# Kernel tuning notes

Measured on AMD Instinct MI355X. Metric: run time of the kernel, lower is better.

## Reference

```python
import jax, jax.numpy as jnp
import numpy as np

DIM = 768
HEADS = 12
HEAD_DIM = DIM // HEADS


def setup_inputs() -> dict:
    key = jax.random.key(0)
    ks = jax.random.split(key, 5)
    s = 0.02
    return {
        "x": jax.random.normal(ks[0], (2, 4096, DIM), dtype=jnp.float32),
        "w_qkv": jax.random.normal(ks[1], (DIM, 3 * DIM), dtype=jnp.float32) * s,
        "b_qkv": jax.random.normal(ks[2], (3 * DIM,), dtype=jnp.float32) * s,
        "w_proj": jax.random.normal(ks[3], (DIM, DIM), dtype=jnp.float32) * s,
        "b_proj": jax.random.normal(ks[4], (DIM,), dtype=jnp.float32) * s,
    }


def reference(x, w_qkv, b_qkv, w_proj, b_proj):
    B, N, _ = x.shape
    scale = HEAD_DIM ** (-0.5)
    qkv = x @ w_qkv + b_qkv                              # [B, N, 3*DIM]
    q, k, v = jnp.split(qkv, 3, axis=-1)
    # 'b n (h d) -> b h n d'
    def to_heads(t):
        return t.reshape(B, N, HEADS, HEAD_DIM).transpose(0, 2, 1, 3)
    q, k, v = to_heads(q), to_heads(k), to_heads(v)
    attn = jnp.einsum('bhnd,bhmd->bhnm', q, k) * scale   # [B, H, N, N]
    attn = jax.nn.softmax(attn, axis=-1)
    out = jnp.einsum('bhnm,bhmd->bhnd', attn, v)         # [B, H, N, D]
    out = out.transpose(0, 2, 1, 3).reshape(B, N, DIM)   # 'b h n d -> b n (h d)'
    return out @ w_proj + b_proj
```

## Files before the change

kernel.cpp:

```cpp
#include <hip/hip_runtime.h>
#include <hip/hip_bf16.h>
#include <stdint.h>

typedef _Float16 f16x8 __attribute__((ext_vector_type(8)));
typedef _Float16 f16x4 __attribute__((ext_vector_type(4)));
typedef uint32_t u32x2 __attribute__((ext_vector_type(2)));
typedef float floatx4 __attribute__((ext_vector_type(4)));

#define NSEQ 4096
#define DIMM 768
#define NHEADS 12
#define HD 64

__device__ __forceinline__ void gload_lds16(const void* g, void* l) {
  typedef __attribute__((address_space(1))) const uint32_t GQ;
  typedef __attribute__((address_space(3))) uint32_t LQ;
  __builtin_amdgcn_global_load_lds((GQ*)g, (LQ*)l, 16, 0, 0);
}

__device__ __forceinline__ uint16_t f16_bits(float v) {
  _Float16 h = (_Float16)v;
  return __builtin_bit_cast(uint16_t, h);
}

__device__ __forceinline__ uint32_t pkrtz(float a, float b) {
  return __builtin_bit_cast(uint32_t, __builtin_amdgcn_cvt_pkrtz(a, b));
}

__device__ __forceinline__ int swz(int row, int e) {
  return row * 64 + ((((e >> 3) ^ (row & 7)) << 3) | (e & 7));
}

__global__ __launch_bounds__(256) void convert_f32_f16(
    const float4* __restrict__ src, f16x8* __restrict__ dst, int n8) {
  const int i = blockIdx.x * 256 + threadIdx.x;
  if (i >= n8) return;
  const float4 a = src[2 * i], b = src[2 * i + 1];
  f16x8 o;
  o[0] = (_Float16)a.x; o[1] = (_Float16)a.y; o[2] = (_Float16)a.z; o[3] = (_Float16)a.w;
  o[4] = (_Float16)b.x; o[5] = (_Float16)b.y; o[6] = (_Float16)b.z; o[7] = (_Float16)b.w;
  dst[i] = o;
}

__global__ __launch_bounds__(256) void transpose_f32_f16(
    const float* __restrict__ src, uint16_t* __restrict__ dst, int R, int C) {
  __shared__ uint16_t tile[32][33];
  const int c0 = blockIdx.x * 32, r0 = blockIdx.y * 32;
  const int tx = threadIdx.x, ty = threadIdx.y;
#pragma unroll
  for (int i = 0; i < 32; i += 8)
    tile[ty + i][tx] = f16_bits(src[(size_t)(r0 + ty + i) * C + (c0 + tx)]);
  __syncthreads();
#pragma unroll
  for (int i = 0; i < 32; i += 8)
    dst[(size_t)(c0 + ty + i) * R + (r0 + tx)] = tile[tx][ty + i];
}

__global__ __launch_bounds__(256) void transpose_b16(
    const uint16_t* __restrict__ src, uint16_t* __restrict__ dst, int R, int C) {
  __shared__ uint16_t tile[32][33];
  const size_t plane = (size_t)blockIdx.z * (size_t)R * (size_t)C;
  const int c0 = blockIdx.x * 32, r0 = blockIdx.y * 32;
  const int tx = threadIdx.x, ty = threadIdx.y;
#pragma unroll
  for (int i = 0; i < 32; i += 8)
    tile[ty + i][tx] = src[plane + (size_t)(r0 + ty + i) * C + (c0 + tx)];
  __syncthreads();
#pragma unroll
  for (int i = 0; i < 32; i += 8)
    dst[plane + (size_t)(c0 + ty + i) * R + (r0 + tx)] = tile[tx][ty + i];
}

__global__ __launch_bounds__(256) void gemm_bt(
    const _Float16* __restrict__ A, const _Float16* __restrict__ Bt,
    const float* __restrict__ bias, int K, int mode,
    void* __restrict__ o0, _Float16* __restrict__ o1, _Float16* __restrict__ o2) {
  __shared__ __attribute__((aligned(16))) _Float16 As[128 * 32];
  __shared__ __attribute__((aligned(16))) _Float16 Bs[128 * 32];
  __shared__ float bias_s[128];
  const int tid = threadIdx.x;
  const int wv = tid >> 6;
  const int lane = tid & 63;
  const int quad = lane >> 4, l16 = lane & 15;
  const int wm = (wv >> 1) * 64, wn = (wv & 1) * 64;
  const int m0 = blockIdx.y * 128, n0 = blockIdx.x * 128;

  if (tid < 128) bias_s[tid] = bias[n0 + tid];

  floatx4 acc[4][4];
#pragma unroll
  for (int i = 0; i < 4; ++i)
#pragma unroll
    for (int j = 0; j < 4; ++j) acc[i][j] = (floatx4){0.f, 0.f, 0.f, 0.f};

  const int gr = lane >> 2, gc = (lane & 3) * 8;
  const _Float16* Ag = A + (size_t)(m0 + wv * 32 + gr) * K + gc;
  const _Float16* Bg = Bt + (size_t)(n0 + wv * 32 + gr) * K + gc;
  const size_t K16 = (size_t)16 * K;
  _Float16* As0 = &As[wv * 1024];
  _Float16* Bs0 = &Bs[wv * 1024];

  for (int kt = 0; kt < K; kt += 32) {
    __syncthreads();
    gload_lds16(Ag + kt, As0);
    gload_lds16(Ag + kt + K16, As0 + 512);
    gload_lds16(Bg + kt, Bs0);
    gload_lds16(Bg + kt + K16, Bs0 + 512);
    __syncthreads();
    f16x8 af[4], bfr[4];
#pragma unroll
    for (int i = 0; i < 4; ++i)
      af[i] = *(const f16x8*)&As[(wm + i * 16 + l16) * 32 + quad * 8];
#pragma unroll
    for (int j = 0; j < 4; ++j)
      bfr[j] = *(const f16x8*)&Bs[(wn + j * 16 + l16) * 32 + quad * 8];
#pragma unroll
    for (int i = 0; i < 4; ++i)
#pragma unroll
      for (int j = 0; j < 4; ++j)
        acc[i][j] = __builtin_amdgcn_mfma_f32_16x16x32_f16(af[i], bfr[j], acc[i][j], 0, 0, 0);
  }

  if (mode == 0) {
    float* of = (float*)o0;
#pragma unroll
    for (int i = 0; i < 4; ++i)
#pragma unroll
      for (int j = 0; j < 4; ++j) {
        const int col = n0 + wn + j * 16 + l16;
        const float b = bias_s[wn + j * 16 + l16];
        const int mrow = m0 + wm + i * 16 + quad * 4;
#pragma unroll
        for (int r = 0; r < 4; ++r)
          of[(size_t)(mrow + r) * DIMM + col] = acc[i][j][r] + b;
      }
  } else {
    const int sec = n0 / DIMM;
    _Float16* dst = (sec == 0) ? (_Float16*)o0 : (sec == 1) ? o1 : o2;
    const float sc = (sec == 0) ? 0.18033688011112042f : 1.0f;
#pragma unroll
    for (int i = 0; i < 4; ++i)
#pragma unroll
      for (int j = 0; j < 4; ++j) {
        const int n = n0 + wn + j * 16 + l16;
        const int c = n - sec * DIMM;
        const int h = c >> 6, d = c & 63;
        const float b = bias_s[wn + j * 16 + l16];
        const int mrow = m0 + wm + i * 16 + quad * 4;
#pragma unroll
        for (int r = 0; r < 4; ++r) {
          const int m = mrow + r;
          const int bb = m >> 12, nr = m & 4095;
          dst[(((size_t)(bb * NHEADS + h)) * NSEQ + nr) * HD + d] =
              (_Float16)((acc[i][j][r] + b) * sc);
        }
      }
  }
}

__global__ __launch_bounds__(256, 3) void attn(
    const _Float16* __restrict__ Qg, const _Float16* __restrict__ Kg,
    const _Float16* __restrict__ VTg, _Float16* __restrict__ ctx) {
  __shared__ __attribute__((aligned(16))) _Float16 Pt[128 * 64];
  __shared__ __attribute__((aligned(16))) _Float16 Ks[2][64 * 64];
  __shared__ __attribute__((aligned(16))) _Float16 VTs[2][64 * 64];
  const int tid = threadIdx.x;
  const int wv = tid >> 6, lane = tid & 63;
  const int quad = lane >> 4, l16 = lane & 15;
  const int bi = blockIdx.x;
  const int xcd = bi & 7, j = bi >> 3;
  const int bh = xcd * 3 + (j >> 5);
  const int q0 = (j & 31) * 128;
  const int bb = bh / NHEADS, h = bh - bb * NHEADS;
  const _Float16* Qp = Qg + (size_t)bh * NSEQ * HD;
  const _Float16* Kp = Kg + (size_t)bh * NSEQ * HD;
  const _Float16* VTp = VTg + (size_t)bh * HD * NSEQ;

  const int krow = tid >> 3;
  const int kcol = (((tid & 7) ^ ((tid >> 3) & 7)) * 8);
  const int l7 = l16 & 7;

#pragma unroll
  for (int i = 0; i < 4; ++i)
    gload_lds16(Qp + (size_t)(q0 + i * 32 + krow) * HD + kcol, &Pt[(i * 256 + wv * 64) * 8]);
#pragma unroll
  for (int i = 0; i < 2; ++i) {
    gload_lds16(Kp + (size_t)(i * 32 + krow) * HD + kcol, &Ks[0][(i * 256 + wv * 64) * 8]);
    gload_lds16(VTp + (size_t)(i * 32 + krow) * NSEQ + kcol, &VTs[0][(i * 256 + wv * 64) * 8]);
  }
  __syncthreads();

  f16x8 aq[2][2];
#pragma unroll
  for (int it = 0; it < 2; ++it)
#pragma unroll
    for (int ks = 0; ks < 2; ++ks)
      aq[it][ks] = *(const f16x8*)&Pt[swz(wv * 32 + it * 16 + l16, ks * 32 + quad * 8)];

  floatx4 o[2][4];
  float lp[2] = {0.f, 0.f};
#pragma unroll
  for (int it = 0; it < 2; ++it)
#pragma unroll
    for (int jn = 0; jn < 4; ++jn) o[it][jn] = (floatx4){0.f, 0.f, 0.f, 0.f};

  const int prow = wv * 32 + l16;

  auto region = [&](const _Float16* bK, const _Float16* bV, _Float16* wK, _Float16* wV, int kvn) {
    __syncthreads();
#pragma unroll
    for (int i = 0; i < 2; ++i) {
      gload_lds16(Kp + (size_t)(kvn + i * 32 + krow) * HD + kcol, &wK[(i * 256 + wv * 64) * 8]);
      gload_lds16(VTp + (size_t)(i * 32 + krow) * NSEQ + kvn + kcol, &wV[(i * 256 + wv * 64) * 8]);
    }
    floatx4 s[2][4];
#pragma unroll
    for (int it = 0; it < 2; ++it)
#pragma unroll
      for (int im = 0; im < 4; ++im) s[it][im] = (floatx4){0.f, 0.f, 0.f, 0.f};
    __builtin_amdgcn_s_setprio(1);
#pragma unroll
    for (int ks = 0; ks < 2; ++ks) {
#pragma unroll
      for (int im = 0; im < 4; ++im) {
        const f16x8 bk = *(const f16x8*)&bK[swz(im * 16 + l16, ks * 32 + quad * 8)];
        s[0][im] = __builtin_amdgcn_mfma_f32_16x16x32_f16(bk, aq[0][ks], s[0][im], 0, 0, 0);
        s[1][im] = __builtin_amdgcn_mfma_f32_16x16x32_f16(bk, aq[1][ks], s[1][im], 0, 0, 0);
      }
    }
    __builtin_amdgcn_s_setprio(0);
#pragma unroll
    for (int it = 0; it < 2; ++it) {
      const int row = prow + it * 16;
#pragma unroll
      for (int im = 0; im < 4; ++im) {
        float p0 = __builtin_amdgcn_exp2f(s[it][im][0]);
        float p1 = __builtin_amdgcn_exp2f(s[it][im][1]);
        float p2 = __builtin_amdgcn_exp2f(s[it][im][2]);
        float p3 = __builtin_amdgcn_exp2f(s[it][im][3]);
        lp[it] += (p0 + p1) + (p2 + p3);
        const u32x2 packed = {pkrtz(p0, p1), pkrtz(p2, p3)};
        *(f16x4*)&Pt[row * 64 + (((im * 2 + (quad >> 1)) ^ l7) << 3) + (quad & 1) * 4] =
            __builtin_bit_cast(f16x4, packed);
      }
    }
    __builtin_amdgcn_s_setprio(1);
#pragma unroll
    for (int kk = 0; kk < 2; ++kk) {
      const f16x8 ap0 = *(const f16x8*)&Pt[swz(prow, kk * 32 + quad * 8)];
      const f16x8 ap1 = *(const f16x8*)&Pt[swz(prow + 16, kk * 32 + quad * 8)];
#pragma unroll
      for (int jn = 0; jn < 4; ++jn) {
        const f16x8 bv = *(const f16x8*)&bV[swz(jn * 16 + l16, kk * 32 + quad * 8)];
        o[0][jn] = __builtin_amdgcn_mfma_f32_16x16x32_f16(ap0, bv, o[0][jn], 0, 0, 0);
        o[1][jn] = __builtin_amdgcn_mfma_f32_16x16x32_f16(ap1, bv, o[1][jn], 0, 0, 0);
      }
    }
    __builtin_amdgcn_s_setprio(0);
  };

#pragma unroll 1
  for (int p = 0; p < 32; ++p) {
    const int t = 2 * p;
    region(Ks[0], VTs[0], Ks[1], VTs[1], ((t + 1) & 63) * 64);
    region(Ks[1], VTs[1], Ks[0], VTs[0], ((t + 2) & 63) * 64);
  }

#pragma unroll
  for (int it = 0; it < 2; ++it) {
    lp[it] += __shfl_xor(lp[it], 16);
    lp[it] += __shfl_xor(lp[it], 32);
  }
#pragma unroll
  for (int it = 0; it < 2; ++it)
#pragma unroll
    for (int r = 0; r < 4; ++r) {
      const int q = q0 + wv * 32 + it * 16 + quad * 4 + r;
      const float lq = __shfl(lp[it], (lane & 48) | (quad * 4 + r));
      const float inv = 1.0f / lq;
      _Float16* dst = ctx + (size_t)(bb * NSEQ + q) * DIMM + h * HD;
#pragma unroll
      for (int jn = 0; jn < 4; ++jn)
        dst[jn * 16 + l16] = (_Float16)(o[it][jn][r] * inv);
    }
}

extern "C" void kernel_launch(void* const* d_in, const int* in_sizes, int n_in,
                              void* d_out, int out_size, void* d_ws, size_t ws_size,
                              hipStream_t stream) {
  char* ws = (char*)d_ws;
  _Float16* xc = (_Float16*)ws;      ws += (size_t)8192 * 768 * 2;
  _Float16* wqkvT = (_Float16*)ws;   ws += (size_t)2304 * 768 * 2;
  _Float16* wprojT = (_Float16*)ws;  ws += (size_t)768 * 768 * 2;
  const size_t qkv_elems = (size_t)2 * NHEADS * NSEQ * HD;
  _Float16* Qb = (_Float16*)ws;      ws += qkv_elems * 2;
  _Float16* Kb = (_Float16*)ws;      ws += qkv_elems * 2;
  _Float16* Vb = (_Float16*)ws;      ws += qkv_elems * 2;
  _Float16* VTb = (_Float16*)ws;     ws += qkv_elems * 2;
  _Float16* ctx = xc;

  const dim3 tb(32, 8, 1);
  const dim3 b256(256, 1, 1);
  hipLaunchKernelGGL(convert_f32_f16, dim3(3072, 1, 1), b256, 0, stream,
                     (const float4*)d_in[0], (f16x8*)xc, 8192 * 768 / 8);
  hipLaunchKernelGGL(transpose_f32_f16, dim3(72, 24, 1), tb, 0, stream,
                     (const float*)d_in[1], (uint16_t*)wqkvT, 768, 2304);
  hipLaunchKernelGGL(transpose_f32_f16, dim3(24, 24, 1), tb, 0, stream,
                     (const float*)d_in[3], (uint16_t*)wprojT, 768, 768);
  hipLaunchKernelGGL(gemm_bt, dim3(18, 64, 1), b256, 0, stream,
                     xc, wqkvT, (const float*)d_in[2], 768, 1, (void*)Qb, Kb, Vb);
  hipLaunchKernelGGL(transpose_b16, dim3(2, 128, 24), tb, 0, stream,
                     (const uint16_t*)Vb, (uint16_t*)VTb, 4096, 64);
  hipLaunchKernelGGL(attn, dim3(768, 1, 1), b256, 0, stream, Qb, Kb, VTb, ctx);
  hipLaunchKernelGGL(gemm_bt, dim3(6, 64, 1), b256, 0, stream,
                     ctx, wprojT, (const float*)d_in[4], 768, 0, d_out,
                     (_Float16*)nullptr, (_Float16*)nullptr);
}
```

Baseline: 292.3 us.

## Software-pipeline attention loop to overlap QK^T with PV of previous tile

Restructures the flash-attention inner loop so each iteration computes S=QK^T for the current KV tile while also running the PV MFMAs for the previous tile's probabilities. The V operands for a tile are preloaded into registers right after the softmax, and the K/V loads for tile 1 are issued before the loop. A prologue for tile 0 and an epilogue PV for the last tile are added. The aim is to cut the serial dependency between exp/softmax and the MFMA phases, at the cost of more live registers (vr, ap, s).

```diff
diff --git a/kernel.cpp b/kernel.cpp
--- a/kernel.cpp
+++ b/kernel.cpp
@@ -197,6 +197,12 @@
     for (int ks = 0; ks < 2; ++ks)
       aq[it][ks] = *(const f16x8*)&Pt[swz(wv * 32 + it * 16 + l16, ks * 32 + quad * 8)];
 
+#pragma unroll
+  for (int i = 0; i < 2; ++i) {
+    gload_lds16(Kp + (size_t)(64 + i * 32 + krow) * HD + kcol, &Ks[1][(i * 256 + wv * 64) * 8]);
+    gload_lds16(VTp + (size_t)(i * 32 + krow) * NSEQ + 64 + kcol, &VTs[1][(i * 256 + wv * 64) * 8]);
+  }
+
   floatx4 o[2][4];
   float lp[2] = {0.f, 0.f};
 #pragma unroll
@@ -205,20 +211,9 @@
     for (int jn = 0; jn < 4; ++jn) o[it][jn] = (floatx4){0.f, 0.f, 0.f, 0.f};
 
   const int prow = wv * 32 + l16;
-
-  auto region = [&](const _Float16* bK, const _Float16* bV, _Float16* wK, _Float16* wV, int kvn) {
-    __syncthreads();
-#pragma unroll
-    for (int i = 0; i < 2; ++i) {
-      gload_lds16(Kp + (size_t)(kvn + i * 32 + krow) * HD + kcol, &wK[(i * 256 + wv * 64) * 8]);
-      gload_lds16(VTp + (size_t)(i * 32 + krow) * NSEQ + kvn + kcol, &wV[(i * 256 + wv * 64) * 8]);
-    }
-    floatx4 s[2][4];
-#pragma unroll
-    for (int it = 0; it < 2; ++it)
-#pragma unroll
-      for (int im = 0; im < 4; ++im) s[it][im] = (floatx4){0.f, 0.f, 0.f, 0.f};
-    __builtin_amdgcn_s_setprio(1);
+  f16x8 vr[2][4];
+
+  auto QKT = [&](const _Float16* bK, floatx4 (&s)[2][4]) {
 #pragma unroll
     for (int ks = 0; ks < 2; ++ks) {
 #pragma unroll
@@ -228,7 +223,15 @@
         s[1][im] = __builtin_amdgcn_mfma_f32_16x16x32_f16(bk, aq[1][ks], s[1][im], 0, 0, 0);
       }
     }
-    __builtin_amdgcn_s_setprio(0);
+  };
+  auto LDVR = [&](const _Float16* bV) {
+#pragma unroll
+    for (int kk = 0; kk < 2; ++kk)
+#pragma unroll
+      for (int jn = 0; jn < 4; ++jn)
+        vr[kk][jn] = *(const f16x8*)&bV[swz(jn * 16 + l16, kk * 32 + quad * 8)];
+  };
+  auto SMAX = [&](floatx4 (&s)[2][4]) {
 #pragma unroll
     for (int it = 0; it < 2; ++it) {
       const int row = prow + it * 16;
@@ -244,26 +247,74 @@
             __builtin_bit_cast(f16x4, packed);
       }
     }
+  };
+  auto LDAP = [&](f16x8 (&ap)[2][2]) {
+#pragma unroll
+    for (int kk = 0; kk < 2; ++kk) {
+      ap[kk][0] = *(const f16x8*)&Pt[swz(prow, kk * 32 + quad * 8)];
+      ap[kk][1] = *(const f16x8*)&Pt[swz(prow + 16, kk * 32 + quad * 8)];
+    }
+  };
+  auto PV = [&](const f16x8 (&ap)[2][2]) {
+#pragma unroll
+    for (int kk = 0; kk < 2; ++kk) {
+#pragma unroll
+      for (int jn = 0; jn < 4; ++jn) {
+        o[0][jn] = __builtin_amdgcn_mfma_f32_16x16x32_f16(ap[kk][0], vr[kk][jn], o[0][jn], 0, 0, 0);
+        o[1][jn] = __builtin_amdgcn_mfma_f32_16x16x32_f16(ap[kk][1], vr[kk][jn], o[1][jn], 0, 0, 0);
+      }
+    }
+  };
+
+  {
+    floatx4 s[2][4];
+#pragma unroll
+    for (int it = 0; it < 2; ++it)
+#pragma unroll
+      for (int im = 0; im < 4; ++im) s[it][im] = (floatx4){0.f, 0.f, 0.f, 0.f};
     __builtin_amdgcn_s_setprio(1);
-#pragma unroll
-    for (int kk = 0; kk < 2; ++kk) {
-      const f16x8 ap0 = *(const f16x8*)&Pt[swz(prow, kk * 32 + quad * 8)];
-      const f16x8 ap1 = *(const f16x8*)&Pt[swz(prow + 16, kk * 32 + quad * 8)];
-#pragma unroll
-      for (int jn = 0; jn < 4; ++jn) {
-        const f16x8 bv = *(const f16x8*)&bV[swz(jn * 16 + l16, kk * 32 + quad * 8)];
-        o[0][jn] = __builtin_amdgcn_mfma_f32_16x16x32_f16(ap0, bv, o[0][jn], 0, 0, 0);
-        o[1][jn] = __builtin_amdgcn_mfma_f32_16x16x32_f16(ap1, bv, o[1][jn], 0, 0, 0);
-      }
-    }
+    QKT(Ks[0], s);
     __builtin_amdgcn_s_setprio(0);
+    LDVR(VTs[0]);
+    SMAX(s);
+  }
+
+  auto REGION = [&](const _Float16* bK, const _Float16* bV,
+                    _Float16* wK, _Float16* wV, int kvn, bool dodma) {
+    __syncthreads();
+    if (dodma) {
+#pragma unroll
+      for (int i = 0; i < 2; ++i) {
+        gload_lds16(Kp + (size_t)(kvn + i * 32 + krow) * HD + kcol, &wK[(i * 256 + wv * 64) * 8]);
+        gload_lds16(VTp + (size_t)(i * 32 + krow) * NSEQ + kvn + kcol, &wV[(i * 256 + wv * 64) * 8]);
+      }
+    }
+    f16x8 ap[2][2];
+    LDAP(ap);
+    floatx4 s[2][4];
+#pragma unroll
+    for (int it = 0; it < 2; ++it)
+#pragma unroll
+      for (int im = 0; im < 4; ++im) s[it][im] = (floatx4){0.f, 0.f, 0.f, 0.f};
+    __builtin_amdgcn_s_setprio(1);
+    QKT(bK, s);
+    PV(ap);
+    __builtin_amdgcn_s_setprio(0);
+    LDVR(bV);
+    SMAX(s);
   };
 
 #pragma unroll 1
-  for (int p = 0; p < 32; ++p) {
-    const int t = 2 * p;
-    region(Ks[0], VTs[0], Ks[1], VTs[1], ((t + 1) & 63) * 64);
-    region(Ks[1], VTs[1], Ks[0], VTs[0], ((t + 2) & 63) * 64);
+  for (int p = 0; p < 31; ++p) {
+    const int t0 = 2 * p + 1;
+    REGION(Ks[1], VTs[1], Ks[0], VTs[0], (t0 + 1) * 64, true);
+    REGION(Ks[0], VTs[0], Ks[1], VTs[1], (t0 + 2) * 64, true);
+  }
+  REGION(Ks[1], VTs[1], Ks[0], VTs[0], 0, false);
+  {
+    f16x8 ap[2][2];
+    LDAP(ap);
+    PV(ap);
   }
 
 #pragma unroll
```

Measured after the change: 281.8 us. -3.6%, faster.
